# Optimization experiments

Measured on AMD Instinct MI355X. Metric: run time of the kernel, lower is better.

Reference implementation:

```python
import jax, jax.numpy as jnp
import numpy as np

HIDDEN = 2048
HEADS = 16
HEAD_DIM = HIDDEN // HEADS  # 128
THETA = 10000.0


def _rope_cache(seq_len, dim, theta=THETA):
    inv_freq = 1.0 / (theta ** (jnp.arange(0, dim, 2, dtype=jnp.float32) / dim))
    t = jnp.arange(seq_len, dtype=jnp.float32)
    freqs = jnp.outer(t, inv_freq)            # [S, dim/2]
    emb = jnp.concatenate([freqs, freqs], -1)  # [S, dim]
    return jnp.cos(emb), jnp.sin(emb)


def _rotate_half(x):
    x1, x2 = jnp.split(x, 2, axis=-1)
    return jnp.concatenate([-x2, x1], axis=-1)


def setup_inputs() -> dict:
    key = jax.random.key(0)
    ks = jax.random.split(key, 5)
    B, S = 2, 2048
    scale = 1.0 / np.sqrt(HIDDEN)
    return {
        "hidden_states": jax.random.normal(ks[0], (B, S, HIDDEN), jnp.float32),
        "wq": jax.random.normal(ks[1], (HIDDEN, HIDDEN), jnp.float32) * scale,
        "wk": jax.random.normal(ks[2], (HIDDEN, HIDDEN), jnp.float32) * scale,
        "wv": jax.random.normal(ks[3], (HIDDEN, HIDDEN), jnp.float32) * scale,
        "wo": jax.random.normal(ks[4], (HIDDEN, HIDDEN), jnp.float32) * scale,
    }


def reference(hidden_states, wq, wk, wv, wo):
    B, S, D = hidden_states.shape
    H, Hd = HEADS, HEAD_DIM
    # projections (nn.Linear: x @ W^T), reshape to [B, H, S, Hd]
    def proj(w):
        return (hidden_states @ w.T).reshape(B, S, H, Hd).transpose(0, 2, 1, 3)
    q, k, v = proj(wq), proj(wk), proj(wv)
    # RoPE
    cos, sin = _rope_cache(S, Hd)             # [S, Hd]
    q = q * cos + _rotate_half(q) * sin
    k = k * cos + _rotate_half(k) * sin
    # scaled dot-product attention with causal mask
    scores = jnp.einsum("bhqd,bhkd->bhqk", q, k) / jnp.sqrt(jnp.float32(Hd))
    causal = jnp.tril(jnp.ones((S, S), bool))
    scores = jnp.where(causal, scores, -jnp.inf)
    attn = jax.nn.softmax(scores, axis=-1)
    out = jnp.einsum("bhqk,bhkd->bhqd", attn, v)  # [B, H, S, Hd]
    out = out.transpose(0, 2, 1, 3).reshape(B, S, D)
    return out @ wo.T
```

## Files before the change

kernel.cpp:

```cpp
#include <hip/hip_runtime.h>
#include <hip/hip_bf16.h>

#define S_LEN  2048
#define BATCH  2
#define NH     16
#define HD     128
#define HIDDEN 2048
#define MROWS  (BATCH*S_LEN)

typedef __attribute__((ext_vector_type(8))) short bf16x8;
typedef __attribute__((ext_vector_type(4))) short s16x4;
typedef __attribute__((ext_vector_type(4))) float f32x4;

__device__ __forceinline__ float bf2f(short s) {
    union { float f; unsigned int u; } v;
    v.u = ((unsigned int)(unsigned short)s) << 16;
    return v.f;
}
__device__ __forceinline__ short f2bf(float f) {
    union { float f; unsigned int u; } v;
    v.f = f;
    unsigned int r = v.u + 0x7fffu + ((v.u >> 16) & 1u);
    return (short)(r >> 16);
}
__device__ __forceinline__ f32x4 mfma16(bf16x8 a, bf16x8 b, f32x4 c) {
    return __builtin_amdgcn_mfma_f32_16x16x32_bf16(a, b, c, 0, 0, 0);
}
__device__ __forceinline__ void gload16(const void* g, void* l) {
    __builtin_amdgcn_global_load_lds(
        (const __attribute__((address_space(1))) void*)g,
        (__attribute__((address_space(3))) void*)l, 16, 0, 0);
}

#define SEG (4194304)
__global__ void cast_k(const float* hs, const float* wq, const float* wk,
                       const float* wv, const float* wo, short* dst)
{
    size_t i = ((size_t)blockIdx.x * 256 + threadIdx.x) * 8;
    int seg = (int)(i >> 22);
    const float* s;
    size_t off;
    if (seg < 2)      { s = hs; off = i; }
    else if (seg == 2){ s = wq; off = i - 2 * (size_t)SEG; }
    else if (seg == 3){ s = wk; off = i - 3 * (size_t)SEG; }
    else if (seg == 4){ s = wv; off = i - 4 * (size_t)SEG; }
    else              { s = wo; off = i - 5 * (size_t)SEG; }
    f32x4 lo = *(const f32x4*)(s + off);
    f32x4 hi = *(const f32x4*)(s + off + 4);
    short v[8];
#pragma unroll
    for (int j = 0; j < 4; ++j) { v[j] = f2bf(lo[j]); v[4 + j] = f2bf(hi[j]); }
    *(bf16x8*)(dst + i) = *(bf16x8*)v;
}

template<int MODE>
__global__ __launch_bounds__(256, 4)
void gemm_bt(const short* A, const short* W0, const short* W1, const short* W2,
             short* Oq, short* Ok, short* Ov, float* Of)
{
    __shared__ short smem[2 * 128 * 64];
    short* As = smem;
    short* Bs = smem + 128 * 64;

    const int tid  = threadIdx.x;
    const int lane = tid & 63;
    const int wv   = tid >> 6;
    const int wr   = wv >> 1, wc = wv & 1;
    const int fr   = lane & 15, fg = lane >> 4;

    const int mt = blockIdx.x;
    int nt = blockIdx.y;
    const short* W = W0;
    short* Ob = Oq;
    int osel = 0;
    if (MODE == 0) {
        osel = nt >> 4; nt &= 15;
        W  = (osel == 0) ? W0 : (osel == 1) ? W1 : W2;
        Ob = (osel == 0) ? Oq : (osel == 1) ? Ok : Ov;
    }
    const int row0 = mt * 128, col0 = nt * 128;
    const int sr = tid >> 3, sb = tid & 7;

    f32x4 acc[4][4];
#pragma unroll
    for (int m = 0; m < 4; ++m)
#pragma unroll
        for (int n = 0; n < 4; ++n) acc[m][n] = (f32x4){0.f, 0.f, 0.f, 0.f};

    for (int k0 = 0; k0 < HIDDEN; k0 += 64) {
        __syncthreads();
#pragma unroll
        for (int it = 0; it < 4; ++it) {
            int r = it * 32 + sr;
            gload16(A + (size_t)(row0 + r) * HIDDEN + k0 + ((sb ^ (r & 7)) * 8),
                    (char*)As + (it * 256 + wv * 64) * 16);
        }
#pragma unroll
        for (int it = 0; it < 4; ++it) {
            int r = it * 32 + sr;
            gload16(W + (size_t)(col0 + r) * HIDDEN + k0 + ((sb ^ (r & 7)) * 8),
                    (char*)Bs + (it * 256 + wv * 64) * 16);
        }
        __syncthreads();
#pragma unroll
        for (int ks = 0; ks < 2; ++ks) {
            bf16x8 a[4], b[4];
#pragma unroll
            for (int m = 0; m < 4; ++m) {
                int r = wr * 64 + m * 16 + fr;
                a[m] = *(const bf16x8*)&As[r * 64 + (((ks * 4 + fg) ^ (r & 7)) * 8)];
            }
#pragma unroll
            for (int n = 0; n < 4; ++n) {
                int r = wc * 64 + n * 16 + fr;
                b[n] = *(const bf16x8*)&Bs[r * 64 + (((ks * 4 + fg) ^ (r & 7)) * 8)];
            }
#pragma unroll
            for (int m = 0; m < 4; ++m)
#pragma unroll
                for (int n = 0; n < 4; ++n)
                    acc[m][n] = mfma16(a[m], b[n], acc[m][n]);
        }
    }

    if (MODE == 0 && osel == 2) {
        __syncthreads();
#pragma unroll
        for (int m = 0; m < 4; ++m)
#pragma unroll
            for (int j = 0; j < 4; ++j) {
                int row = wr * 64 + m * 16 + fg * 4 + j;
#pragma unroll
                for (int n = 0; n < 4; ++n) {
                    int col = wc * 64 + n * 16 + fr;
                    smem[col * 128 + (((row >> 3) ^ (col & 15)) * 8) + (row & 7)] =
                        f2bf(acc[m][n][j]);
                }
            }
        __syncthreads();
        const int b_ = row0 >> 11;
        const int bh = b_ * NH + nt;
        const int s0 = row0 & (S_LEN - 1);
#pragma unroll
        for (int it = 0; it < 8; ++it) {
            int c = it * 256 + tid;
            int d = c >> 4, sbk = c & 15;
            bf16x8 vv = *(const bf16x8*)&smem[d * 128 + ((sbk ^ (d & 15)) * 8)];
            *(bf16x8*)(Ov + ((size_t)bh * HD + d) * S_LEN + s0 + sbk * 8) = vv;
        }
    } else {
#pragma unroll
        for (int m = 0; m < 4; ++m)
#pragma unroll
            for (int j = 0; j < 4; ++j) {
                int mrow = row0 + wr * 64 + m * 16 + fg * 4 + j;
#pragma unroll
                for (int n = 0; n < 4; ++n) {
                    int col = col0 + wc * 64 + n * 16 + fr;
                    float val = acc[m][n][j];
                    if (MODE == 0) {
                        int b_ = mrow >> 11, s = mrow & (S_LEN - 1);
                        int h = col >> 7, d = col & (HD - 1);
                        Ob[((size_t)(b_ * NH + h) * S_LEN + s) * HD + d] = f2bf(val);
                    } else {
                        Of[(size_t)mrow * HIDDEN + col] = val;
                    }
                }
            }
    }
}

__global__ void rope_table_k(float* tab)
{
    int i = blockIdx.x * 256 + threadIdx.x;
    if (i >= S_LEN * 64) return;
    int s = i >> 6, d = i & 63;
    float inv = 1.0f / powf(10000.0f, (float)d * (1.0f / 64.0f));
    float ang = (float)s * inv;
    tab[2 * i]     = cosf(ang);
    tab[2 * i + 1] = sinf(ang);
}

__global__ void rope_apply_k(short* Q, short* K, const float* tab)
{
    int i = blockIdx.x * 256 + threadIdx.x;
    int d8 = i & 7;
    int s  = (i >> 3) & (S_LEN - 1);
    int bh = i >> 14;
    size_t base = ((size_t)bh * S_LEN + s) * HD + d8 * 8;
    const float* tp = tab + (s * 64 + d8 * 8) * 2;
    f32x4 t[4];
#pragma unroll
    for (int j = 0; j < 4; ++j) t[j] = *(const f32x4*)(tp + j * 4);

    bf16x8 q1 = *(bf16x8*)(Q + base), q2 = *(bf16x8*)(Q + base + 64);
    bf16x8 k1 = *(bf16x8*)(K + base), k2 = *(bf16x8*)(K + base + 64);
    short oq1[8], oq2[8], ok1[8], ok2[8];
    const float qs = 0.08838834764831845f;
#pragma unroll
    for (int j = 0; j < 8; ++j) {
        float c  = t[j >> 1][(j & 1) * 2];
        float sn = t[j >> 1][(j & 1) * 2 + 1];
        float a1 = bf2f(q1[j]), a2 = bf2f(q2[j]);
        oq1[j] = f2bf((a1 * c - a2 * sn) * qs);
        oq2[j] = f2bf((a2 * c + a1 * sn) * qs);
        float b1 = bf2f(k1[j]), b2 = bf2f(k2[j]);
        ok1[j] = f2bf(b1 * c - b2 * sn);
        ok2[j] = f2bf(b2 * c + b1 * sn);
    }
    *(bf16x8*)(Q + base)      = *(bf16x8*)oq1;
    *(bf16x8*)(Q + base + 64) = *(bf16x8*)oq2;
    *(bf16x8*)(K + base)      = *(bf16x8*)ok1;
    *(bf16x8*)(K + base + 64) = *(bf16x8*)ok2;
}

__global__ __launch_bounds__(256, 1)
void attn_k(const short* Q, const short* K, const short* Vt, short* AO)
{
    __shared__ short Ks[2][64 * 128];
    __shared__ short Vs[2][128 * 64];
    __shared__ short Ps[4][32 * 64];

    const int tid = threadIdx.x, lane = tid & 63, wv = tid >> 6;
    const int fr = lane & 15, fg = lane >> 4;
    const int bh = blockIdx.x & 31;
    const int p  = blockIdx.x >> 5;

    const short* Qb = Q  + (size_t)bh * S_LEN * HD;
    const short* Kb = K  + (size_t)bh * S_LEN * HD;
    const short* Vb = Vt + (size_t)bh * HD * S_LEN;
    const int b_ = bh >> 4, h = bh & 15;

#define STAGE(t, bufi)                                                          \
    do {                                                                        \
        const int kb_ = (t) * 64;                                               \
        _Pragma("unroll")                                                       \
        for (int i_ = 0; i_ < 4; ++i_) {                                        \
            int c_ = i_ * 256 + tid;                                            \
            int r_ = c_ >> 4, bb_ = c_ & 15;                                    \
            gload16(Kb + (size_t)(kb_ + r_) * HD + ((bb_ ^ (r_ & 15)) * 8),     \
                    (char*)&Ks[bufi][0] + (i_ * 256 + wv * 64) * 16);           \
        }                                                                       \
        _Pragma("unroll")                                                       \
        for (int i_ = 0; i_ < 4; ++i_) {                                        \
            int c_ = i_ * 256 + tid;                                            \
            int r_ = c_ >> 3, bb_ = c_ & 7;                                     \
            gload16(Vb + (size_t)r_ * S_LEN + kb_ + ((bb_ ^ (r_ & 7)) * 8),     \
                    (char*)&Vs[bufi][0] + (i_ * 256 + wv * 64) * 16);           \
        }                                                                       \
    } while (0)

#pragma unroll 1
    for (int phase = 0; phase < 2; ++phase) {
        const int qt = phase ? (15 - p) : p;
        const int qbase = qt * 128 + wv * 32;

        bf16x8 qf[2][4];
#pragma unroll
        for (int mi = 0; mi < 2; ++mi)
#pragma unroll
            for (int ks = 0; ks < 4; ++ks)
                qf[mi][ks] = *(const bf16x8*)(Qb + (size_t)(qbase + mi * 16 + fr) * HD
                                              + ks * 32 + fg * 8);

        f32x4 oT[2][8];
        float mrun[2], lrun[2];
#pragma unroll
        for (int mi = 0; mi < 2; ++mi) {
#pragma unroll
            for (int nd = 0; nd < 8; ++nd) oT[mi][nd] = (f32x4){0.f, 0.f, 0.f, 0.f};
            mrun[mi] = -1e30f;
            lrun[mi] = 0.f;
        }

        const int ntiles = (qt + 1) * 2;
        __syncthreads();
        STAGE(0, 0);

        for (int t = 0; t < ntiles; ++t) {
            const int buf = t & 1;
            __syncthreads();
            if (t + 1 < ntiles) STAGE(t + 1, buf ^ 1);
            const int kb = t * 64;

            if (kb <= qbase + 31) {
                f32x4 sc[4][2];
#pragma unroll
                for (int ni = 0; ni < 4; ++ni)
#pragma unroll
                    for (int mi = 0; mi < 2; ++mi) sc[ni][mi] = (f32x4){0.f, 0.f, 0.f, 0.f};
#pragma unroll
                for (int ks = 0; ks < 4; ++ks) {
                    bf16x8 kf[4];
#pragma unroll
                    for (int ni = 0; ni < 4; ++ni) {
                        int kc = ni * 16 + fr;
                        kf[ni] = *(const bf16x8*)&Ks[buf][kc * 128 + (((ks * 4 + fg) ^ (kc & 15)) * 8)];
                    }
#pragma unroll
                    for (int ni = 0; ni < 4; ++ni)
#pragma unroll
                        for (int mi = 0; mi < 2; ++mi)
                            sc[ni][mi] = mfma16(kf[ni], qf[mi][ks], sc[ni][mi]);
                }
                const bool need_mask = (kb + 63 > qbase);
#pragma unroll
                for (int mi = 0; mi < 2; ++mi) {
                    const int qrow = qbase + mi * 16 + fr;
                    if (need_mask) {
#pragma unroll
                        for (int ni = 0; ni < 4; ++ni)
#pragma unroll
                            for (int j = 0; j < 4; ++j) {
                                int kcol = kb + ni * 16 + fg * 4 + j;
                                if (kcol > qrow) sc[ni][mi][j] = -1e30f;
                            }
                    }
                    float mx = sc[0][mi][0];
#pragma unroll
                    for (int ni = 0; ni < 4; ++ni)
#pragma unroll
                        for (int j = 0; j < 4; ++j)
                            mx = fmaxf(mx, sc[ni][mi][j]);
                    mx = fmaxf(mx, __shfl_xor(mx, 16));
                    mx = fmaxf(mx, __shfl_xor(mx, 32));
                    if (mx > mrun[mi]) {
                        float scale = __expf(mrun[mi] - mx);
                        mrun[mi] = mx;
                        lrun[mi] *= scale;
#pragma unroll
                        for (int nd = 0; nd < 8; ++nd) {
#pragma unroll
                            for (int j = 0; j < 4; ++j) oT[mi][nd][j] *= scale;
                        }
                    }
                    const float m_ = mrun[mi];
                    float rs = 0.f;
                    const int q = mi * 16 + fr;
#pragma unroll
                    for (int ni = 0; ni < 4; ++ni) {
                        float e0 = __expf(sc[ni][mi][0] - m_);
                        float e1 = __expf(sc[ni][mi][1] - m_);
                        float e2 = __expf(sc[ni][mi][2] - m_);
                        float e3 = __expf(sc[ni][mi][3] - m_);
                        rs += (e0 + e1) + (e2 + e3);
                        s16x4 w;
                        w[0] = f2bf(e0); w[1] = f2bf(e1);
                        w[2] = f2bf(e2); w[3] = f2bf(e3);
                        int blk = ni * 2 + (fg >> 1);
                        *(s16x4*)&Ps[wv][q * 64 + ((blk ^ (q & 7)) * 8) + (fg & 1) * 4] = w;
                    }
                    rs += __shfl_xor(rs, 16);
                    rs += __shfl_xor(rs, 32);
                    lrun[mi] += rs;
                }
                asm volatile("s_waitcnt lgkmcnt(0)" ::: "memory");
                bf16x8 pf[2][2];
#pragma unroll
                for (int mi = 0; mi < 2; ++mi) {
                    const int q = mi * 16 + fr;
#pragma unroll
                    for (int ks = 0; ks < 2; ++ks)
                        pf[mi][ks] = *(const bf16x8*)&Ps[wv][q * 64 + (((ks * 4 + fg) ^ (q & 7)) * 8)];
                }
#pragma unroll
                for (int nd = 0; nd < 8; ++nd) {
                    const int d = nd * 16 + fr;
#pragma unroll
                    for (int ks = 0; ks < 2; ++ks) {
                        bf16x8 vf = *(const bf16x8*)&Vs[buf][d * 64 + (((ks * 4 + fg) ^ (d & 7)) * 8)];
#pragma unroll
                        for (int mi = 0; mi < 2; ++mi)
                            oT[mi][nd] = mfma16(vf, pf[mi][ks], oT[mi][nd]);
                    }
                }
            }
        }

#pragma unroll
        for (int mi = 0; mi < 2; ++mi) {
            float inv = 1.0f / lrun[mi];
            int srow = qbase + mi * 16 + fr;
#pragma unroll
            for (int nd = 0; nd < 8; ++nd) {
                s16x4 w;
#pragma unroll
                for (int j = 0; j < 4; ++j) w[j] = f2bf(oT[mi][nd][j] * inv);
                *(s16x4*)(AO + ((size_t)b_ * S_LEN + srow) * HIDDEN
                          + h * HD + nd * 16 + fg * 4) = w;
            }
        }
    }
#undef STAGE
}

extern "C" void kernel_launch(void* const* d_in, const int* in_sizes, int n_in,
                              void* d_out, int out_size, void* d_ws, size_t ws_size,
                              hipStream_t stream)
{
    const float* hs = (const float*)d_in[0];
    const float* wq = (const float*)d_in[1];
    const float* wk = (const float*)d_in[2];
    const float* wvp = (const float*)d_in[3];
    const float* wo = (const float*)d_in[4];
    float* out = (float*)d_out;

    char* ws = (char*)d_ws;
    short* CB  = (short*)ws;
    short* Hb  = CB;
    short* Wqb = CB + 2 * (size_t)SEG;
    short* Wkb = CB + 3 * (size_t)SEG;
    short* Wvb = CB + 4 * (size_t)SEG;
    short* Wob = CB + 5 * (size_t)SEG;
    short* Qb  = (short*)(ws + 50331648);
    short* Kb  = (short*)(ws + 67108864);
    short* Vb  = (short*)(ws + 83886080);
    short* AO  = Hb;
    float* tab = (float*)(ws + 100663296);

    cast_k<<<dim3(12288), dim3(256), 0, stream>>>(hs, wq, wk, wvp, wo, CB);
    rope_table_k<<<dim3(512), dim3(256), 0, stream>>>(tab);
    gemm_bt<0><<<dim3(32, 48), dim3(256), 0, stream>>>(
        Hb, Wqb, Wkb, Wvb, Qb, Kb, Vb, nullptr);
    rope_apply_k<<<dim3(2048), dim3(256), 0, stream>>>(Qb, Kb, tab);
    attn_k<<<dim3(256), dim3(256), 0, stream>>>(Qb, Kb, Vb, AO);
    gemm_bt<1><<<dim3(32, 16), dim3(256), 0, stream>>>(
        AO, Wob, nullptr, nullptr, nullptr, nullptr, nullptr, out);
}
```

Before: 376.5 us.

## Keep softmax probabilities in registers and halve per-block query tile in attention

Measured after the change: 355.3 us. 1.06x faster.

```diff
diff --git a/kernel.cpp b/kernel.cpp
--- a/kernel.cpp
+++ b/kernel.cpp
@@ -214,23 +214,26 @@
     *(bf16x8*)(K + base + 64) = *(bf16x8*)ok2;
 }
 
-__global__ __launch_bounds__(256, 1)
+__global__ __launch_bounds__(256, 2)
 void attn_k(const short* Q, const short* K, const short* Vt, short* AO)
 {
     __shared__ short Ks[2][64 * 128];
     __shared__ short Vs[2][128 * 64];
-    __shared__ short Ps[4][32 * 64];
 
     const int tid = threadIdx.x, lane = tid & 63, wv = tid >> 6;
     const int fr = lane & 15, fg = lane >> 4;
-    const int bh = blockIdx.x & 31;
-    const int p  = blockIdx.x >> 5;
+    const int bid = blockIdx.x;
+    const int bh   = bid & 31;
+    const int sub  = bid >> 5;
+    const int p    = sub >> 1;
+    const int half = sub & 1;
 
     const short* Qb = Q  + (size_t)bh * S_LEN * HD;
     const short* Kb = K  + (size_t)bh * S_LEN * HD;
     const short* Vb = Vt + (size_t)bh * HD * S_LEN;
     const int b_ = bh >> 4, h = bh & 15;
 
+#define SWK(r) (((r) & 3) | ((((r) >> 3) & 3) << 2))
 #define STAGE(t, bufi)                                                          \
     do {                                                                        \
         const int kb_ = (t) * 64;                                               \
@@ -238,7 +241,7 @@
         for (int i_ = 0; i_ < 4; ++i_) {                                        \
             int c_ = i_ * 256 + tid;                                            \
             int r_ = c_ >> 4, bb_ = c_ & 15;                                    \
-            gload16(Kb + (size_t)(kb_ + r_) * HD + ((bb_ ^ (r_ & 15)) * 8),     \
+            gload16(Kb + (size_t)(kb_ + r_) * HD + ((bb_ ^ SWK(r_)) * 8),       \
                     (char*)&Ks[bufi][0] + (i_ * 256 + wv * 64) * 16);           \
         }                                                                       \
         _Pragma("unroll")                                                       \
@@ -253,27 +256,20 @@
 #pragma unroll 1
     for (int phase = 0; phase < 2; ++phase) {
         const int qt = phase ? (15 - p) : p;
-        const int qbase = qt * 128 + wv * 32;
-
-        bf16x8 qf[2][4];
-#pragma unroll
-        for (int mi = 0; mi < 2; ++mi)
-#pragma unroll
-            for (int ks = 0; ks < 4; ++ks)
-                qf[mi][ks] = *(const bf16x8*)(Qb + (size_t)(qbase + mi * 16 + fr) * HD
-                                              + ks * 32 + fg * 8);
-
-        f32x4 oT[2][8];
-        float mrun[2], lrun[2];
-#pragma unroll
-        for (int mi = 0; mi < 2; ++mi) {
-#pragma unroll
-            for (int nd = 0; nd < 8; ++nd) oT[mi][nd] = (f32x4){0.f, 0.f, 0.f, 0.f};
-            mrun[mi] = -1e30f;
-            lrun[mi] = 0.f;
-        }
-
-        const int ntiles = (qt + 1) * 2;
+        const int qbase = qt * 128 + half * 64 + wv * 16;
+
+        bf16x8 qf[4];
+#pragma unroll
+        for (int ks = 0; ks < 4; ++ks)
+            qf[ks] = *(const bf16x8*)(Qb + (size_t)(qbase + fr) * HD
+                                      + ks * 32 + fg * 8);
+
+        f32x4 oT[8];
+#pragma unroll
+        for (int nd = 0; nd < 8; ++nd) oT[nd] = (f32x4){0.f, 0.f, 0.f, 0.f};
+        float mrun = -1e30f, lrun = 0.f;
+
+        const int ntiles = qt * 2 + 1 + half;
         __syncthreads();
         STAGE(0, 0);
 
@@ -283,115 +279,94 @@
             if (t + 1 < ntiles) STAGE(t + 1, buf ^ 1);
             const int kb = t * 64;
 
-            if (kb <= qbase + 31) {
-                f32x4 sc[4][2];
-#pragma unroll
-                for (int ni = 0; ni < 4; ++ni)
-#pragma unroll
-                    for (int mi = 0; mi < 2; ++mi) sc[ni][mi] = (f32x4){0.f, 0.f, 0.f, 0.f};
+            if (kb <= qbase + 15) {
+                f32x4 sc[4];
+#pragma unroll
+                for (int ni = 0; ni < 4; ++ni) sc[ni] = (f32x4){0.f, 0.f, 0.f, 0.f};
+                __builtin_amdgcn_s_setprio(1);
 #pragma unroll
                 for (int ks = 0; ks < 4; ++ks) {
                     bf16x8 kf[4];
 #pragma unroll
                     for (int ni = 0; ni < 4; ++ni) {
-                        int kc = ni * 16 + fr;
-                        kf[ni] = *(const bf16x8*)&Ks[buf][kc * 128 + (((ks * 4 + fg) ^ (kc & 15)) * 8)];
+                        int rk = ((ni & 1) << 5) + ((fr >> 2) << 3)
+                               + ((ni >> 1) << 2) + (fr & 3);
+                        kf[ni] = *(const bf16x8*)&Ks[buf][rk * 128
+                                     + (((ks * 4 + fg) ^ fr) * 8)];
                     }
 #pragma unroll
                     for (int ni = 0; ni < 4; ++ni)
-#pragma unroll
-                        for (int mi = 0; mi < 2; ++mi)
-                            sc[ni][mi] = mfma16(kf[ni], qf[mi][ks], sc[ni][mi]);
-                }
-                const bool need_mask = (kb + 63 > qbase);
-#pragma unroll
-                for (int mi = 0; mi < 2; ++mi) {
-                    const int qrow = qbase + mi * 16 + fr;
-                    if (need_mask) {
-#pragma unroll
-                        for (int ni = 0; ni < 4; ++ni)
-#pragma unroll
-                            for (int j = 0; j < 4; ++j) {
-                                int kcol = kb + ni * 16 + fg * 4 + j;
-                                if (kcol > qrow) sc[ni][mi][j] = -1e30f;
-                            }
+                        sc[ni] = mfma16(kf[ni], qf[ks], sc[ni]);
+                }
+                __builtin_amdgcn_s_setprio(0);
+                const int qrow = qbase + fr;
+                if (kb + 63 > qbase) {
+#pragma unroll
+                    for (int ni = 0; ni < 4; ++ni)
+#pragma unroll
+                        for (int j = 0; j < 4; ++j) {
+                            int kcol = kb + ((ni & 1) << 5) + (fg << 3)
+                                     + ((ni >> 1) << 2) + j;
+                            if (kcol > qrow) sc[ni][j] = -1e30f;
+                        }
+                }
+                float mx = sc[0][0];
+#pragma unroll
+                for (int ni = 0; ni < 4; ++ni)
+#pragma unroll
+                    for (int j = 0; j < 4; ++j) mx = fmaxf(mx, sc[ni][j]);
+                mx = fmaxf(mx, __shfl_xor(mx, 16));
+                mx = fmaxf(mx, __shfl_xor(mx, 32));
+                if (mx > mrun) {
+                    float scale = __expf(mrun - mx);
+                    mrun = mx;
+                    lrun *= scale;
+#pragma unroll
+                    for (int nd = 0; nd < 8; ++nd)
+#pragma unroll
+                        for (int j = 0; j < 4; ++j) oT[nd][j] *= scale;
+                }
+                float rs = 0.f;
+                short pw[16];
+#pragma unroll
+                for (int ni = 0; ni < 4; ++ni)
+#pragma unroll
+                    for (int j = 0; j < 4; ++j) {
+                        float pe = __expf(sc[ni][j] - mrun);
+                        rs += pe;
+                        pw[((ni & 1) << 3) + ((ni >> 1) << 2) + j] = f2bf(pe);
                     }
-                    float mx = sc[0][mi][0];
-#pragma unroll
-                    for (int ni = 0; ni < 4; ++ni)
-#pragma unroll
-                        for (int j = 0; j < 4; ++j)
-                            mx = fmaxf(mx, sc[ni][mi][j]);
-                    mx = fmaxf(mx, __shfl_xor(mx, 16));
-                    mx = fmaxf(mx, __shfl_xor(mx, 32));
-                    if (mx > mrun[mi]) {
-                        float scale = __expf(mrun[mi] - mx);
-                        mrun[mi] = mx;
-                        lrun[mi] *= scale;
-#pragma unroll
-                        for (int nd = 0; nd < 8; ++nd) {
-#pragma unroll
-                            for (int j = 0; j < 4; ++j) oT[mi][nd][j] *= scale;
-                        }
-                    }
-                    const float m_ = mrun[mi];
-                    float rs = 0.f;
-                    const int q = mi * 16 + fr;
-#pragma unroll
-                    for (int ni = 0; ni < 4; ++ni) {
-                        float e0 = __expf(sc[ni][mi][0] - m_);
-                        float e1 = __expf(sc[ni][mi][1] - m_);
-                        float e2 = __expf(sc[ni][mi][2] - m_);
-                        float e3 = __expf(sc[ni][mi][3] - m_);
-                        rs += (e0 + e1) + (e2 + e3);
-                        s16x4 w;
-                        w[0] = f2bf(e0); w[1] = f2bf(e1);
-                        w[2] = f2bf(e2); w[3] = f2bf(e3);
-                        int blk = ni * 2 + (fg >> 1);
-                        *(s16x4*)&Ps[wv][q * 64 + ((blk ^ (q & 7)) * 8) + (fg & 1) * 4] = w;
-                    }
-                    rs += __shfl_xor(rs, 16);
-                    rs += __shfl_xor(rs, 32);
-                    lrun[mi] += rs;
-                }
-                asm volatile("s_waitcnt lgkmcnt(0)" ::: "memory");
-                bf16x8 pf[2][2];
-#pragma unroll
-                for (int mi = 0; mi < 2; ++mi) {
-                    const int q = mi * 16 + fr;
-#pragma unroll
-                    for (int ks = 0; ks < 2; ++ks)
-                        pf[mi][ks] = *(const bf16x8*)&Ps[wv][q * 64 + (((ks * 4 + fg) ^ (q & 7)) * 8)];
-                }
+                bf16x8 pf0 = *(bf16x8*)&pw[0];
+                bf16x8 pf1 = *(bf16x8*)&pw[8];
+                rs += __shfl_xor(rs, 16);
+                rs += __shfl_xor(rs, 32);
+                lrun += rs;
+                __builtin_amdgcn_s_setprio(1);
 #pragma unroll
                 for (int nd = 0; nd < 8; ++nd) {
                     const int d = nd * 16 + fr;
-#pragma unroll
-                    for (int ks = 0; ks < 2; ++ks) {
-                        bf16x8 vf = *(const bf16x8*)&Vs[buf][d * 64 + (((ks * 4 + fg) ^ (d & 7)) * 8)];
-#pragma unroll
-                        for (int mi = 0; mi < 2; ++mi)
-                            oT[mi][nd] = mfma16(vf, pf[mi][ks], oT[mi][nd]);
-                    }
-                }
+                    bf16x8 vf0 = *(const bf16x8*)&Vs[buf][d * 64 + ((fg ^ (d & 7)) * 8)];
+                    bf16x8 vf1 = *(const bf16x8*)&Vs[buf][d * 64 + (((4 + fg) ^ (d & 7)) * 8)];
+                    oT[nd] = mfma16(vf0, pf0, oT[nd]);
+                    oT[nd] = mfma16(vf1, pf1, oT[nd]);
+                }
+                __builtin_amdgcn_s_setprio(0);
             }
         }
 
-#pragma unroll
-        for (int mi = 0; mi < 2; ++mi) {
-            float inv = 1.0f / lrun[mi];
-            int srow = qbase + mi * 16 + fr;
-#pragma unroll
-            for (int nd = 0; nd < 8; ++nd) {
-                s16x4 w;
-#pragma unroll
-                for (int j = 0; j < 4; ++j) w[j] = f2bf(oT[mi][nd][j] * inv);
-                *(s16x4*)(AO + ((size_t)b_ * S_LEN + srow) * HIDDEN
-                          + h * HD + nd * 16 + fg * 4) = w;
-            }
+        float inv = 1.0f / lrun;
+        int srow = qbase + fr;
+#pragma unroll
+        for (int nd = 0; nd < 8; ++nd) {
+            s16x4 w;
+#pragma unroll
+            for (int j = 0; j < 4; ++j) w[j] = f2bf(oT[nd][j] * inv);
+            *(s16x4*)(AO + ((size_t)b_ * S_LEN + srow) * HIDDEN
+                      + h * HD + nd * 16 + fg * 4) = w;
         }
     }
 #undef STAGE
+#undef SWK
 }
 
 extern "C" void kernel_launch(void* const* d_in, const int* in_sizes, int n_in,
@@ -423,7 +398,7 @@
     gemm_bt<0><<<dim3(32, 48), dim3(256), 0, stream>>>(
         Hb, Wqb, Wkb, Wvb, Qb, Kb, Vb, nullptr);
     rope_apply_k<<<dim3(2048), dim3(256), 0, stream>>>(Qb, Kb, tab);
-    attn_k<<<dim3(256), dim3(256), 0, stream>>>(Qb, Kb, Vb, AO);
+    attn_k<<<dim3(512), dim3(256), 0, stream>>>(Qb, Kb, Vb, AO);
     gemm_bt<1><<<dim3(32, 16), dim3(256), 0, stream>>>(
         AO, Wob, nullptr, nullptr, nullptr, nullptr, nullptr, out);
 }
```
